# Kernel tuning notes

Hardware: AMD Instinct MI355X
Metric: run time of the kernel (lower is better)

The kernel has to match this reference:

```python
import jax, jax.numpy as jnp
import numpy as np

B = 4096      # batch
OBS = 512     # observation dim
T = 10        # num_tasks
E = 8         # num_experts
W = 1024      # width
H = 12        # head_dim
EPS = 1e-8


def setup_inputs() -> dict:
    key = jax.random.key(0)
    ks = jax.random.split(key, 8)
    obs = jax.random.normal(ks[0], (B, OBS), jnp.float32)
    task_id = jax.random.randint(ks[1], (B,), 0, T)
    task_onehot = jax.nn.one_hot(task_id, T, dtype=jnp.float32)
    x = jnp.concatenate([obs, task_onehot], axis=-1)  # (B, OBS+T)
    he = lambda k, shape, fan: jax.random.normal(k, shape, jnp.float32) * np.float32(np.sqrt(2.0 / fan))
    te_W = he(ks[2], (T, E), T)               # task-embedding Dense (no bias)
    W0 = he(ks[3], (E, OBS, W), OBS); b0 = jnp.zeros((E, W), jnp.float32)
    W1 = he(ks[4], (E, W, W), W);     b1 = jnp.zeros((E, W), jnp.float32)
    W2 = he(ks[5], (E, W, W), W);     b2 = jnp.zeros((E, W), jnp.float32)
    head_W = he(ks[6], (T, W, H), W); head_b = jnp.zeros((T, H), jnp.float32)
    return dict(x=x, te_W=te_W, W0=W0, b0=b0, W1=W1, b1=b1, W2=W2, b2=b2,
                head_W=head_W, head_b=head_b)


def _gram_schmidt(eo):
    # eo: (B, E, W) -> orthonormal basis (B, E, W), sequential over expert axis
    basis = [eo[:, 0] / (jnp.linalg.norm(eo[:, 0], axis=1, keepdims=True) + EPS)]
    for i in range(1, E):
        Bm = jnp.stack(basis, axis=1)               # (B, i, W)
        v = eo[:, i]                                # (B, W)
        coeff = jnp.einsum('bd,bid->bi', v, Bm)     # projections onto current basis
        w = v - jnp.einsum('bi,bid->bd', coeff, Bm)
        basis.append(w / (jnp.linalg.norm(w, axis=1, keepdims=True) + EPS))
    return jnp.stack(basis, axis=1)


def reference(x, te_W, W0, b0, W1, b1, W2, b2, head_W, head_b):
    task_oh = x[:, -T:]                              # (B, T) one-hot
    obs = x[:, :-T]                                  # (B, OBS)
    te = task_oh @ te_W                              # (B, E) task embedding
    # per-expert MLP (vmapped over experts via stacked weights)
    h = jax.nn.relu(jnp.einsum('bd,edw->bew', obs, W0) + b0)
    h = jax.nn.relu(jnp.einsum('bew,ewv->bev', h, W1) + b1)
    eo = jnp.einsum('bew,ewv->bev', h, W2) + b2      # (B, E, W)
    basis = _gram_schmidt(eo)                        # (B, E, W)
    feat = jnp.tanh(jnp.einsum('bek,be->bk', basis, te))  # (B, W)
    heads = jnp.einsum('bk,tkh->bth', feat, head_W) + head_b  # (B, T, H)
    idx = jnp.argmax(task_oh, axis=-1)
    return heads[jnp.arange(x.shape[0]), idx]        # (B, H)
```

## Files before the change

### kernel.cpp

```cpp
#include <hip/hip_runtime.h>
#include <stdint.h>

#define B_SZ   4096
#define OBS    512
#define T_TASKS 10
#define E_EXP  8
#define W_DIM  1024
#define H_OUT  12
#define XROW   522
#define NTOT   8192

using f32x4  = __attribute__((ext_vector_type(4))) float;
using bf16x8 = __attribute__((ext_vector_type(8))) short;

__device__ __forceinline__ unsigned short f2bf(float f) {
  union { float f; unsigned u; } x; x.f = f;
  unsigned r = x.u + 0x7FFF + ((x.u >> 16) & 1);
  return (unsigned short)(r >> 16);
}
__device__ __forceinline__ float bf2f(unsigned short h) {
  union { unsigned u; float f; } x; x.u = ((unsigned)h) << 16;
  return x.f;
}

__device__ __forceinline__ void gload_lds16(const void* g, void* l) {
  __builtin_amdgcn_global_load_lds(
      (const __attribute__((address_space(1))) void*)g,
      (__attribute__((address_space(3))) void*)l,
      16, 0, 0);
}

#define VMCNT4  do { asm volatile("s_waitcnt vmcnt(4)" ::: "memory"); \
                     __builtin_amdgcn_sched_barrier(0); } while (0)
#define BARRIER do { asm volatile("s_barrier" ::: "memory"); \
                     __builtin_amdgcn_sched_barrier(0); } while (0)
#define SCHED0  __builtin_amdgcn_sched_barrier(0)


__global__ void k_obs_bf16(const float* __restrict__ x, unsigned short* __restrict__ obsB) {
  int i = blockIdx.x * 256 + threadIdx.x;
  int b = i >> 9, c = i & 511;
  obsB[i] = f2bf(x[(size_t)b * XROW + c]);
}

__global__ void k_wt(const float* __restrict__ Wsrc, unsigned short* __restrict__ Wt, int K) {
  __shared__ float tile[32][33];
  int e  = blockIdx.z;
  int n0 = blockIdx.x * 32, k0 = blockIdx.y * 32;
  const float* Ws = Wsrc + (size_t)e * K * W_DIM;
  unsigned short* Wd = Wt + (size_t)e * W_DIM * K;
  int tx = threadIdx.x & 31, ty = threadIdx.x >> 5;
#pragma unroll
  for (int r = 0; r < 4; ++r)
    tile[ty + r * 8][tx] = Ws[(size_t)(k0 + ty + r * 8) * W_DIM + n0 + tx];
  __syncthreads();
#pragma unroll
  for (int r = 0; r < 4; ++r)
    Wd[(size_t)(n0 + ty + r * 8) * K + k0 + tx] = f2bf(tile[tx][ty + r * 8]);
}


template <bool RELU>
__global__ __launch_bounds__(512, 2) void k_gemm256(
    const unsigned short* __restrict__ A, int lda, int aExpStride,
    const unsigned short* __restrict__ Bt, int K,
    const float* __restrict__ bias,
    unsigned short* __restrict__ C)
{
  extern __shared__ char lds[];
  const int tid  = threadIdx.x;
  const int lane = tid & 63, wid = tid >> 6;
  const int wm = wid >> 2, wn = wid & 3;
  const int rlo = lane & 15, kg = lane >> 4;

  int bid = blockIdx.x;
  int xcd = bid & 7, loc = bid >> 3;
  int mblk = ((xcd & 1) << 3) | (loc & 7);
  int nblk = ((xcd >> 1) << 3) | (loc >> 3);
  int m0 = mblk * 256, n0g = nblk * 256;
  int e = n0g >> 10, n0e = n0g & 1023;

  const unsigned short* Ab = A + (size_t)e * aExpStride;
  const unsigned short* Bb = Bt + ((size_t)e * 1024 + n0e) * (size_t)K;

  const int idx0 = tid, idx1 = 512 + tid;
  const int r0 = idx0 >> 3, p0 = idx0 & 7, c0 = p0 ^ (r0 & 7);
  const int r1 = idx1 >> 3, p1 = idx1 & 7, c1 = p1 ^ (r1 & 7);

  const int NT = K >> 6;
  const size_t ldaz = (size_t)lda, ldkz = (size_t)K;

  auto stageA = [&](int buf, int h, int kt) {
    const unsigned short* g0 = Ab + (size_t)(m0 + h * 128 + r0) * ldaz + kt * 64 + c0 * 8;
    const unsigned short* g1 = Ab + (size_t)(m0 + h * 128 + r1) * ldaz + kt * 64 + c1 * 8;
    char* l = lds + buf * 65536 + h * 16384;
    gload_lds16(g0, l + idx0 * 16);
    gload_lds16(g1, l + idx1 * 16);
  };
  auto stageB = [&](int buf, int h, int kt) {
    const unsigned short* g0 = Bb + (size_t)(h * 128 + r0) * ldkz + kt * 64 + c0 * 8;
    const unsigned short* g1 = Bb + (size_t)(h * 128 + r1) * ldkz + kt * 64 + c1 * 8;
    char* l = lds + buf * 65536 + 32768 + h * 16384;
    gload_lds16(g0, l + idx0 * 16);
    gload_lds16(g1, l + idx1 * 16);
  };
  auto rdA = [&](int buf, int mh, int mi, int ks) -> bf16x8 {
    int r = mi * 32 + wm * 16 + rlo;
    int p = (ks * 4 + kg) ^ (r & 7);
    return *(const bf16x8*)(lds + buf * 65536 + mh * 16384 + r * 128 + p * 16);
  };
  auto rdB = [&](int buf, int nh, int ni, int ks) -> bf16x8 {
    int r = ni * 64 + wn * 16 + rlo;
    int p = (ks * 4 + kg) ^ (r & 7);
    return *(const bf16x8*)(lds + buf * 65536 + 32768 + nh * 16384 + r * 128 + p * 16);
  };

  f32x4 acc[8][4];
#pragma unroll
  for (int i = 0; i < 8; ++i)
#pragma unroll
    for (int j = 0; j < 4; ++j) acc[i][j] = f32x4{0.f, 0.f, 0.f, 0.f};

  bf16x8 af[8], bf0[4], bf1[4];

  stageA(0, 0, 0); stageB(0, 0, 0); stageB(0, 1, 0); stageA(0, 1, 0);
  stageA(1, 0, (1 < NT - 1) ? 1 : NT - 1);
  asm volatile("s_waitcnt vmcnt(6)" ::: "memory");
  SCHED0;
  BARRIER;
#pragma unroll
  for (int mi = 0; mi < 4; ++mi)
#pragma unroll
    for (int ks = 0; ks < 2; ++ks) af[mi * 2 + ks] = rdA(0, 0, mi, ks);
#pragma unroll
  for (int ni = 0; ni < 2; ++ni)
#pragma unroll
    for (int ks = 0; ks < 2; ++ks) bf0[ni * 2 + ks] = rdB(0, 0, ni, ks);

  for (int t = 0; t < NT; ++t) {
    int buf = t & 1, nbuf = buf ^ 1;
    int tn  = (t + 1 < NT) ? t + 1 : NT - 1;
    int tn2 = (t + 2 < NT) ? t + 2 : NT - 1;

    VMCNT4;
    BARRIER;
#pragma unroll
    for (int ni = 0; ni < 2; ++ni)
#pragma unroll
      for (int ks = 0; ks < 2; ++ks) bf1[ni * 2 + ks] = rdB(buf, 1, ni, ks);
    stageB(nbuf, 0, tn);
    SCHED0;
    __builtin_amdgcn_s_setprio(1);
#pragma unroll
    for (int ks = 0; ks < 2; ++ks)
#pragma unroll
      for (int mi = 0; mi < 4; ++mi)
#pragma unroll
        for (int ni = 0; ni < 2; ++ni)
          acc[mi][ni] = __builtin_amdgcn_mfma_f32_16x16x32_bf16(af[mi * 2 + ks], bf0[ni * 2 + ks], acc[mi][ni], 0, 0, 0);
    __builtin_amdgcn_s_setprio(0);
    SCHED0;

    VMCNT4;
    BARRIER;
    stageB(nbuf, 1, tn);
    SCHED0;
    __builtin_amdgcn_s_setprio(1);
#pragma unroll
    for (int ks = 0; ks < 2; ++ks)
#pragma unroll
      for (int mi = 0; mi < 4; ++mi)
#pragma unroll
        for (int ni = 0; ni < 2; ++ni)
          acc[mi][2 + ni] = __builtin_amdgcn_mfma_f32_16x16x32_bf16(af[mi * 2 + ks], bf1[ni * 2 + ks], acc[mi][2 + ni], 0, 0, 0);
    __builtin_amdgcn_s_setprio(0);
    SCHED0;
#pragma unroll
    for (int mi = 0; mi < 4; ++mi)
#pragma unroll
      for (int ks = 0; ks < 2; ++ks) af[mi * 2 + ks] = rdA(buf, 1, mi, ks);

    VMCNT4;
    BARRIER;
    stageA(nbuf, 1, tn);
    SCHED0;
    __builtin_amdgcn_s_setprio(1);
#pragma unroll
    for (int ks = 0; ks < 2; ++ks)
#pragma unroll
      for (int mi = 0; mi < 4; ++mi)
#pragma unroll
        for (int ni = 0; ni < 2; ++ni)
          acc[4 + mi][2 + ni] = __builtin_amdgcn_mfma_f32_16x16x32_bf16(af[mi * 2 + ks], bf1[ni * 2 + ks], acc[4 + mi][2 + ni], 0, 0, 0);
    __builtin_amdgcn_s_setprio(0);
    SCHED0;

    VMCNT4;
    BARRIER;
    stageA(buf, 0, tn2);
    SCHED0;
    __builtin_amdgcn_s_setprio(1);
#pragma unroll
    for (int ks = 0; ks < 2; ++ks)
#pragma unroll
      for (int mi = 0; mi < 4; ++mi)
#pragma unroll
        for (int ni = 0; ni < 2; ++ni)
          acc[4 + mi][ni] = __builtin_amdgcn_mfma_f32_16x16x32_bf16(af[mi * 2 + ks], bf0[ni * 2 + ks], acc[4 + mi][ni], 0, 0, 0);
    __builtin_amdgcn_s_setprio(0);
    SCHED0;
#pragma unroll
    for (int mi = 0; mi < 4; ++mi)
#pragma unroll
      for (int ks = 0; ks < 2; ++ks) af[mi * 2 + ks] = rdA(nbuf, 0, mi, ks);
#pragma unroll
    for (int ni = 0; ni < 2; ++ni)
#pragma unroll
      for (int ks = 0; ks < 2; ++ks) bf0[ni * 2 + ks] = rdB(nbuf, 0, ni, ks);
  }

  int rbase = kg * 4;
#pragma unroll
  for (int fi = 0; fi < 8; ++fi) {
    int mh = fi >> 2, mi = fi & 3;
    int rowg = m0 + mh * 128 + mi * 32 + wm * 16 + rbase;
#pragma unroll
    for (int fj = 0; fj < 4; ++fj) {
      int nh = fj >> 1, ni = fj & 1;
      int colr = nh * 128 + ni * 64 + wn * 16 + rlo;
      int colg = n0g + colr;
      float bv = bias[e * W_DIM + n0e + colr];
#pragma unroll
      for (int j = 0; j < 4; ++j) {
        float v = acc[fi][fj][j] + bv;
        if (RELU) v = fmaxf(v, 0.0f);
        C[(size_t)(rowg + j) * NTOT + colg] = f2bf(v);
      }
    }
  }
}


__device__ __forceinline__ float wred(float s) {
#pragma unroll
  for (int m = 32; m; m >>= 1) s += __shfl_xor(s, m, 64);
  return s;
}

__global__ __launch_bounds__(256, 1) void k_gs_wave(
    const unsigned short* __restrict__ eo,
    const float* __restrict__ x,
    const float* __restrict__ te_W,
    const float* __restrict__ head_W,
    const float* __restrict__ head_b,
    float* __restrict__ out)
{
  int wid = threadIdx.x >> 6, lane = threadIdx.x & 63;
  int b = blockIdx.x * 4 + wid;

  float v[8][16];
  const unsigned short* row = eo + (size_t)b * NTOT;
#pragma unroll
  for (int i = 0; i < E_EXP; ++i) {
#pragma unroll
    for (int half = 0; half < 2; ++half) {
      bf16x8 t = *(const bf16x8*)&row[i * 1024 + half * 512 + lane * 8];
#pragma unroll
      for (int k = 0; k < 8; ++k) v[i][half * 8 + k] = bf2f((unsigned short)t[k]);
    }
  }

  int idx = 0; float mv = x[(size_t)b * XROW + OBS];
#pragma unroll
  for (int t = 1; t < T_TASKS; ++t) {
    float val = x[(size_t)b * XROW + OBS + t];
    if (val > mv) { mv = val; idx = t; }
  }

  float cf[7];
#pragma unroll
  for (int i = 0; i < E_EXP; ++i) {
#pragma unroll
    for (int j = 0; j < 7; ++j) {
      if (j < i) {
        float p = 0.f;
#pragma unroll
        for (int c = 0; c < 16; ++c) p += v[i][c] * v[j][c];
        cf[j] = wred(p);
      }
    }
#pragma unroll
    for (int c = 0; c < 16; ++c) {
      float w = v[i][c];
#pragma unroll
      for (int j = 0; j < 7; ++j)
        if (j < i) w -= cf[j] * v[j][c];
      v[i][c] = w;
    }
    float p = 0.f;
#pragma unroll
    for (int c = 0; c < 16; ++c) p += v[i][c] * v[i][c];
    float nrm = sqrtf(wred(p));
    float s = 1.0f / (nrm + 1e-8f);
#pragma unroll
    for (int c = 0; c < 16; ++c) v[i][c] *= s;
  }

  float te[E_EXP];
#pragma unroll
  for (int e2 = 0; e2 < E_EXP; ++e2) te[e2] = te_W[idx * E_EXP + e2];

  float ph[H_OUT];
#pragma unroll
  for (int h = 0; h < H_OUT; ++h) ph[h] = 0.f;
  const float* hw = head_W + (size_t)idx * W_DIM * H_OUT;

#pragma unroll
  for (int half = 0; half < 2; ++half) {
#pragma unroll
    for (int k = 0; k < 8; ++k) {
      int c = half * 512 + lane * 8 + k;
      float f = 0.f;
#pragma unroll
      for (int e2 = 0; e2 < E_EXP; ++e2) f += te[e2] * v[e2][half * 8 + k];
      f = tanhf(f);
      const float* hwc = hw + (size_t)c * H_OUT;
#pragma unroll
      for (int h = 0; h < H_OUT; ++h) ph[h] += f * hwc[h];
    }
  }

#pragma unroll
  for (int h = 0; h < H_OUT; ++h) ph[h] = wred(ph[h]);
  if (lane == 0) {
#pragma unroll
    for (int h = 0; h < H_OUT; ++h)
      out[(size_t)b * H_OUT + h] = ph[h] + head_b[idx * H_OUT + h];
  }
}


extern "C" void kernel_launch(void* const* d_in, const int* in_sizes, int n_in,
                              void* d_out, int out_size, void* d_ws, size_t ws_size,
                              hipStream_t stream) {
  const float* x     = (const float*)d_in[0];
  const float* te_W  = (const float*)d_in[1];
  const float* W0    = (const float*)d_in[2];
  const float* b0    = (const float*)d_in[3];
  const float* W1    = (const float*)d_in[4];
  const float* b1    = (const float*)d_in[5];
  const float* W2    = (const float*)d_in[6];
  const float* b2    = (const float*)d_in[7];
  const float* headW = (const float*)d_in[8];
  const float* headb = (const float*)d_in[9];
  float* out = (float*)d_out;

  char* ws = (char*)d_ws;
  size_t off = 0;
  auto alloc = [&](size_t bytes) {
    void* p = ws + off;
    off += (bytes + 255) & ~(size_t)255;
    return p;
  };
  unsigned short* obsB = (unsigned short*)alloc((size_t)B_SZ * OBS * 2);
  unsigned short* W0t  = (unsigned short*)alloc((size_t)8 * 1024 * 512 * 2);
  unsigned short* W1t  = (unsigned short*)alloc((size_t)8 * 1024 * 1024 * 2);
  unsigned short* W2t  = (unsigned short*)alloc((size_t)8 * 1024 * 1024 * 2);
  unsigned short* h0   = (unsigned short*)alloc((size_t)B_SZ * NTOT * 2);
  unsigned short* h1   = (unsigned short*)alloc((size_t)B_SZ * NTOT * 2);
  unsigned short* eo   = (unsigned short*)alloc((size_t)B_SZ * NTOT * 2);
  (void)ws_size; (void)in_sizes; (void)n_in; (void)out_size;

  k_obs_bf16<<<(B_SZ * OBS) / 256, 256, 0, stream>>>(x, obsB);
  k_wt<<<dim3(32, 16, 8), 256, 0, stream>>>(W0, W0t, 512);
  k_wt<<<dim3(32, 32, 8), 256, 0, stream>>>(W1, W1t, 1024);
  k_wt<<<dim3(32, 32, 8), 256, 0, stream>>>(W2, W2t, 1024);

  k_gemm256<true ><<<512, 512, 131072, stream>>>(obsB, 512,  0,    W0t, 512,  b0, h0);
  k_gemm256<true ><<<512, 512, 131072, stream>>>(h0,   NTOT, 1024, W1t, 1024, b1, h1);
  k_gemm256<false><<<512, 512, 131072, stream>>>(h1,   NTOT, 1024, W2t, 1024, b2, eo);

  k_gs_wave<<<B_SZ / 4, 256, 0, stream>>>(eo, x, te_W, headW, headb, out);
}
```

Baseline: 245.3 us.

## Restructure GEMM main loop into deeper prefetch with per-phase LDS barriers

Reworks the 256x256 bf16 MFMA GEMM pipeline so the prologue stages a full extra tile (both A and B halves of tile 1), and each of the four MFMA phases reads its fragments from the current buffer, issues a global->LDS stage for a future tile, then barriers and waits on LDS counts. The vmcnt wait moves to once per iteration (vmcnt 6) instead of four times, and barriers are added after each MFMA block to protect buffer reuse. The goal is to keep more global loads in flight and reduce stalls on memory, at the cost of more barriers per iteration and a changed buffer-overwrite ordering that must stay race-free.

Measured after the change: 253.6 us. 1.03x slower.

```diff
diff --git a/kernel.cpp b/kernel.cpp
--- a/kernel.cpp
+++ b/kernel.cpp
@@ -30,11 +30,10 @@
       16, 0, 0);
 }
 
-#define VMCNT4  do { asm volatile("s_waitcnt vmcnt(4)" ::: "memory"); \
-                     __builtin_amdgcn_sched_barrier(0); } while (0)
-#define BARRIER do { asm volatile("s_barrier" ::: "memory"); \
-                     __builtin_amdgcn_sched_barrier(0); } while (0)
 #define SCHED0  __builtin_amdgcn_sched_barrier(0)
+#define VMCNT6  do { asm volatile("s_waitcnt vmcnt(6)" ::: "memory"); SCHED0; } while (0)
+#define LGKM0   do { asm volatile("s_waitcnt lgkmcnt(0)" ::: "memory"); SCHED0; } while (0)
+#define BARRIER do { SCHED0; asm volatile("s_barrier" ::: "memory"); SCHED0; } while (0)
 
 
 __global__ void k_obs_bf16(const float* __restrict__ x, unsigned short* __restrict__ obsB) {
@@ -123,33 +122,30 @@
 
   bf16x8 af[8], bf0[4], bf1[4];
 
-  stageA(0, 0, 0); stageB(0, 0, 0); stageB(0, 1, 0); stageA(0, 1, 0);
-  stageA(1, 0, (1 < NT - 1) ? 1 : NT - 1);
-  asm volatile("s_waitcnt vmcnt(6)" ::: "memory");
-  SCHED0;
-  BARRIER;
-#pragma unroll
-  for (int mi = 0; mi < 4; ++mi)
-#pragma unroll
-    for (int ks = 0; ks < 2; ++ks) af[mi * 2 + ks] = rdA(0, 0, mi, ks);
-#pragma unroll
-  for (int ni = 0; ni < 2; ++ni)
-#pragma unroll
-    for (int ks = 0; ks < 2; ++ks) bf0[ni * 2 + ks] = rdB(0, 0, ni, ks);
+  {
+    int t1 = NT > 1 ? 1 : 0;
+    stageA(0, 0, 0); stageB(0, 0, 0); stageB(0, 1, 0); stageA(0, 1, 0);
+    stageA(1, 0, t1); stageB(1, 0, t1); stageB(1, 1, t1);
+    VMCNT6;
+    BARRIER;
+  }
 
   for (int t = 0; t < NT; ++t) {
     int buf = t & 1, nbuf = buf ^ 1;
     int tn  = (t + 1 < NT) ? t + 1 : NT - 1;
     int tn2 = (t + 2 < NT) ? t + 2 : NT - 1;
 
-    VMCNT4;
-    BARRIER;
+#pragma unroll
+    for (int mi = 0; mi < 4; ++mi)
+#pragma unroll
+      for (int ks = 0; ks < 2; ++ks) af[mi * 2 + ks] = rdA(buf, 0, mi, ks);
 #pragma unroll
     for (int ni = 0; ni < 2; ++ni)
 #pragma unroll
-      for (int ks = 0; ks < 2; ++ks) bf1[ni * 2 + ks] = rdB(buf, 1, ni, ks);
-    stageB(nbuf, 0, tn);
-    SCHED0;
+      for (int ks = 0; ks < 2; ++ks) bf0[ni * 2 + ks] = rdB(buf, 0, ni, ks);
+    stageA(nbuf, 1, tn);
+    BARRIER;
+    LGKM0;
     __builtin_amdgcn_s_setprio(1);
 #pragma unroll
     for (int ks = 0; ks < 2; ++ks)
@@ -159,12 +155,15 @@
         for (int ni = 0; ni < 2; ++ni)
           acc[mi][ni] = __builtin_amdgcn_mfma_f32_16x16x32_bf16(af[mi * 2 + ks], bf0[ni * 2 + ks], acc[mi][ni], 0, 0, 0);
     __builtin_amdgcn_s_setprio(0);
-    SCHED0;
-
-    VMCNT4;
-    BARRIER;
-    stageB(nbuf, 1, tn);
-    SCHED0;
+    BARRIER;
+
+#pragma unroll
+    for (int ni = 0; ni < 2; ++ni)
+#pragma unroll
+      for (int ks = 0; ks < 2; ++ks) bf1[ni * 2 + ks] = rdB(buf, 1, ni, ks);
+    stageA(buf, 0, tn2);
+    BARRIER;
+    LGKM0;
     __builtin_amdgcn_s_setprio(1);
 #pragma unroll
     for (int ks = 0; ks < 2; ++ks)
@@ -174,16 +173,15 @@
         for (int ni = 0; ni < 2; ++ni)
           acc[mi][2 + ni] = __builtin_amdgcn_mfma_f32_16x16x32_bf16(af[mi * 2 + ks], bf1[ni * 2 + ks], acc[mi][2 + ni], 0, 0, 0);
     __builtin_amdgcn_s_setprio(0);
-    SCHED0;
+    BARRIER;
+
 #pragma unroll
     for (int mi = 0; mi < 4; ++mi)
 #pragma unroll
       for (int ks = 0; ks < 2; ++ks) af[mi * 2 + ks] = rdA(buf, 1, mi, ks);
-
-    VMCNT4;
-    BARRIER;
-    stageA(nbuf, 1, tn);
-    SCHED0;
+    stageB(buf, 0, tn2);
+    BARRIER;
+    LGKM0;
     __builtin_amdgcn_s_setprio(1);
 #pragma unroll
     for (int ks = 0; ks < 2; ++ks)
@@ -193,12 +191,10 @@
         for (int ni = 0; ni < 2; ++ni)
           acc[4 + mi][2 + ni] = __builtin_amdgcn_mfma_f32_16x16x32_bf16(af[mi * 2 + ks], bf1[ni * 2 + ks], acc[4 + mi][2 + ni], 0, 0, 0);
     __builtin_amdgcn_s_setprio(0);
-    SCHED0;
-
-    VMCNT4;
-    BARRIER;
-    stageA(buf, 0, tn2);
-    SCHED0;
+    BARRIER;
+
+    stageB(buf, 1, tn2);
+    BARRIER;
     __builtin_amdgcn_s_setprio(1);
 #pragma unroll
     for (int ks = 0; ks < 2; ++ks)
@@ -208,16 +204,11 @@
         for (int ni = 0; ni < 2; ++ni)
           acc[4 + mi][ni] = __builtin_amdgcn_mfma_f32_16x16x32_bf16(af[mi * 2 + ks], bf0[ni * 2 + ks], acc[4 + mi][ni], 0, 0, 0);
     __builtin_amdgcn_s_setprio(0);
-    SCHED0;
-#pragma unroll
-    for (int mi = 0; mi < 4; ++mi)
-#pragma unroll
-      for (int ks = 0; ks < 2; ++ks) af[mi * 2 + ks] = rdA(nbuf, 0, mi, ks);
-#pragma unroll
-    for (int ni = 0; ni < 2; ++ni)
-#pragma unroll
-      for (int ks = 0; ks < 2; ++ks) bf0[ni * 2 + ks] = rdB(nbuf, 0, ni, ks);
-  }
+    VMCNT6;
+    BARRIER;
+  }
+  asm volatile("s_waitcnt vmcnt(0)" ::: "memory");
+  SCHED0;
 
   int rbase = kg * 4;
 #pragma unroll
```
